# Kernel optimization log

Measured on AMD Instinct MI355X. Metric: run time of the kernel, lower is better.

The kernel has to match this reference:

```python
import jax, jax.numpy as jnp
import numpy as np

N_NODES = 100000
N_EDGES = 1600000
NUM_GRAPHS = 1000

def gcn_conv(x, edge_index, W, b, n):
    # PyG GCNConv: out = D^-1/2 (A + I) D^-1/2 (x W) + b
    xw = x @ W                                   # [n, F_out]
    loop = jnp.arange(n, dtype=edge_index.dtype)
    src = jnp.concatenate([edge_index[0], loop])  # sources (messages come from src)
    dst = jnp.concatenate([edge_index[1], loop])  # targets (aggregated into dst)
    deg = jnp.zeros((n,), xw.dtype).at[dst].add(1.0)
    dinv = jnp.where(deg > 0, jax.lax.rsqrt(deg), 0.0)
    norm = dinv[src] * dinv[dst]                  # [E+n]
    msg = xw[src] * norm[:, None]                 # gather + scale
    out = jax.ops.segment_sum(msg, dst, num_segments=n)
    return out + b

def scatter_mean(x, seg, num_segments):
    sums = jax.ops.segment_sum(x, seg, num_segments=num_segments)
    cnt = jax.ops.segment_sum(jnp.ones((x.shape[0],), x.dtype), seg, num_segments=num_segments)
    return sums / jnp.maximum(cnt, 1.0)[:, None]

def setup_inputs() -> dict:
    key = jax.random.key(0)
    ks = jax.random.split(key, 9)
    x = jax.random.normal(ks[0], (N_NODES, 256), dtype=jnp.float32)
    edge_index = jax.random.randint(ks[1], (2, N_EDGES), 0, N_NODES, dtype=jnp.int64 if jax.config.jax_enable_x64 else jnp.int32).astype(jnp.int32)
    batch = jnp.sort(jax.random.randint(ks[2], (N_NODES,), 0, NUM_GRAPHS)).astype(jnp.int32)
    W1 = jax.random.normal(ks[3], (256, 128), dtype=jnp.float32) * 0.05
    b1 = jax.random.normal(ks[4], (128,), dtype=jnp.float32) * 0.05
    W2 = jax.random.normal(ks[5], (128, 64), dtype=jnp.float32) * 0.05
    b2 = jax.random.normal(ks[6], (64,), dtype=jnp.float32) * 0.05
    fc_W = jax.random.normal(ks[7], (64, 4), dtype=jnp.float32) * 0.05
    fc_b = jax.random.normal(ks[8], (4,), dtype=jnp.float32) * 0.05
    return {"x": x, "edge_index": edge_index, "batch": batch, "W1": W1, "b1": b1, "W2": W2, "b2": b2, "fc_W": fc_W, "fc_b": fc_b}

def reference(x, edge_index, batch, W1, b1, W2, b2, fc_W, fc_b):
    n = x.shape[0]
    h = gcn_conv(x, edge_index, W1, b1, n)
    h = jax.nn.relu(h)                 # dropout p=0.0 is identity
    h = gcn_conv(h, edge_index, W2, b2, n)
    g = scatter_mean(h, batch, NUM_GRAPHS)   # [G, out_feats]
    logits = g @ fc_W + fc_b
    return jax.nn.log_softmax(logits, axis=1)
```

## Files before the change

### kernel.cpp

```cpp
#include <hip/hip_runtime.h>
#include <hip/hip_bf16.h>

#define N_NODES 100000
#define N_EDGES 1600000
#define NUM_GRAPHS 1000

#define NODES_PER_BUCKET 256
#define BUCKET_SHIFT 8
#define NBUCKETS 391
#define CAP 5120

#define G1_BLOCKS 782
#define FUSED_BLOCKS 1563
#define FILL_CHUNK 2052

typedef __attribute__((ext_vector_type(8))) short short8;
typedef __attribute__((ext_vector_type(4))) float f32x4;
typedef __attribute__((ext_vector_type(2))) float f32x2;
typedef unsigned short ushort;

__device__ __forceinline__ ushort f2bf(float f) {
    unsigned int u = __float_as_uint(f);
    u = u + 0x7fffu + ((u >> 16) & 1u);
    return (ushort)(u >> 16);
}

__device__ __forceinline__ unsigned char f2fp8(float f) {
    return (unsigned char)(__builtin_amdgcn_cvt_pk_fp8_f32(f, f, 0, false) & 0xff);
}

__global__ void setup_kernel(int* __restrict__ bcursor,
                             const float* __restrict__ W1, ushort* __restrict__ W1t,
                             const float* __restrict__ W2, ushort* __restrict__ W2t,
                             float* __restrict__ gsum, float* __restrict__ gcnt) {
    int b = blockIdx.x, tid = threadIdx.x;
    if (b < 2) {
        int i = b * 256 + tid;
        if (i < NBUCKETS) bcursor[i] = i * CAP;
    } else if (b < 130) {
        int idx = (b - 2) * 256 + tid;
        int n = idx & 127, k = idx >> 7;
        W1t[n * 256 + k] = f2bf(W1[k * 128 + n]);
    } else if (b < 162) {
        int idx = (b - 130) * 256 + tid;
        int n = idx & 63, k = idx >> 6;
        W2t[n * 128 + k] = f2bf(W2[k * 64 + n]);
    } else {
        int idx = (b - 162) * 256 + tid;
        if (idx < NUM_GRAPHS * 64) gsum[idx] = 0.f;
        else if (idx < NUM_GRAPHS * 64 + NUM_GRAPHS) gcnt[idx - NUM_GRAPHS * 64] = 0.f;
    }
}
#define SETUP_BLOCKS 416

__global__ __launch_bounds__(256) void gemm1_fill_kernel(const float* __restrict__ x,
                                                         const ushort* __restrict__ W1t,
                                                         unsigned char* __restrict__ outb,
                                                         const int* __restrict__ esrc,
                                                         const int* __restrict__ edst,
                                                         int* __restrict__ bcursor,
                                                         int* __restrict__ pairs) {
    __shared__ short8 Bs[2048];
    const int b = blockIdx.x;
    const int tid = threadIdx.x;

    if (b & 1) {
        int* scnt = (int*)Bs;
        int* spos = scnt + NBUCKETS;
        const int fid = b >> 1;
        const int beg = fid * FILL_CHUNK;
        int end = beg + FILL_CHUNK;
        if (end > N_EDGES) end = N_EDGES;
        if (beg >= end) return;
        for (int i = tid; i < NBUCKETS; i += 256) scnt[i] = 0;
        __syncthreads();
        for (int e = beg + tid * 4; e < end; e += 1024) {
            int4 d4 = *(const int4*)&edst[e];
            atomicAdd(&scnt[d4.x >> BUCKET_SHIFT], 1);
            atomicAdd(&scnt[d4.y >> BUCKET_SHIFT], 1);
            atomicAdd(&scnt[d4.z >> BUCKET_SHIFT], 1);
            atomicAdd(&scnt[d4.w >> BUCKET_SHIFT], 1);
        }
        __syncthreads();
        for (int i = tid; i < NBUCKETS; i += 256) {
            int c = scnt[i];
            spos[i] = c > 0 ? atomicAdd(&bcursor[i], c) : 0;
        }
        __syncthreads();
        for (int e = beg + tid * 4; e < end; e += 1024) {
            int4 d4 = *(const int4*)&edst[e];
            int4 s4 = *(const int4*)&esrc[e];
            int p0 = atomicAdd(&spos[d4.x >> BUCKET_SHIFT], 1);
            pairs[p0] = (s4.x << 8) | (d4.x & 255);
            int p1 = atomicAdd(&spos[d4.y >> BUCKET_SHIFT], 1);
            pairs[p1] = (s4.y << 8) | (d4.y & 255);
            int p2 = atomicAdd(&spos[d4.z >> BUCKET_SHIFT], 1);
            pairs[p2] = (s4.z << 8) | (d4.z & 255);
            int p3 = atomicAdd(&spos[d4.w >> BUCKET_SHIFT], 1);
            pairs[p3] = (s4.w << 8) | (d4.w & 255);
        }
        return;
    }

    const int gid = b >> 1;
    const int row0 = gid * 128;
    const int wv = tid >> 6;
    const int l = tid & 63;
    const int lrow = l & 15;
    const int quad = l >> 4;

    int r0 = row0 + wv * 16 + lrow;
    int r1 = r0 + 64;
    if (r0 > N_NODES - 1) r0 = N_NODES - 1;
    if (r1 > N_NODES - 1) r1 = N_NODES - 1;
    const float* xr0 = x + (size_t)r0 * 256 + quad * 8;
    const float* xr1 = x + (size_t)r1 * 256 + quad * 8;
    const int frag = lrow * 4 + quad;

    f32x4 acc[2][8];
#pragma unroll
    for (int m = 0; m < 2; ++m)
#pragma unroll
        for (int t = 0; t < 8; ++t) acc[m][t] = (f32x4){0.f, 0.f, 0.f, 0.f};

    for (int s = 0; s < 2; ++s) {
        if (s) __syncthreads();
#pragma unroll
        for (int j = 0; j < 8; ++j) {
            int slot = j * 256 + tid;
            int kcl = slot >> 9, t = (slot >> 6) & 7, lr = (slot >> 2) & 15, q = slot & 3;
            Bs[slot] = *(const short8*)(W1t + (t * 16 + lr) * 256 + (s * 4 + kcl) * 32 + q * 8);
        }
        __syncthreads();

#pragma unroll
        for (int kcl = 0; kcl < 4; ++kcl) {
            const int kc = s * 4 + kcl;
            float4 a00 = *(const float4*)(xr0 + kc * 32);
            float4 a01 = *(const float4*)(xr0 + kc * 32 + 4);
            float4 a10 = *(const float4*)(xr1 + kc * 32);
            float4 a11 = *(const float4*)(xr1 + kc * 32 + 4);
            short8 af0, af1;
            af0[0] = (short)f2bf(a00.x); af0[1] = (short)f2bf(a00.y);
            af0[2] = (short)f2bf(a00.z); af0[3] = (short)f2bf(a00.w);
            af0[4] = (short)f2bf(a01.x); af0[5] = (short)f2bf(a01.y);
            af0[6] = (short)f2bf(a01.z); af0[7] = (short)f2bf(a01.w);
            af1[0] = (short)f2bf(a10.x); af1[1] = (short)f2bf(a10.y);
            af1[2] = (short)f2bf(a10.z); af1[3] = (short)f2bf(a10.w);
            af1[4] = (short)f2bf(a11.x); af1[5] = (short)f2bf(a11.y);
            af1[6] = (short)f2bf(a11.z); af1[7] = (short)f2bf(a11.w);
#pragma unroll
            for (int t = 0; t < 8; ++t) {
                short8 bfrag = Bs[kcl * 512 + t * 64 + frag];
                acc[0][t] = __builtin_amdgcn_mfma_f32_16x16x32_bf16(af0, bfrag, acc[0][t], 0, 0, 0);
                acc[1][t] = __builtin_amdgcn_mfma_f32_16x16x32_bf16(af1, bfrag, acc[1][t], 0, 0, 0);
            }
        }
    }

#pragma unroll
    for (int m = 0; m < 2; ++m) {
        const int rbase = row0 + m * 64 + wv * 16 + quad * 4;
#pragma unroll
        for (int t = 0; t < 8; ++t) {
#pragma unroll
            for (int r = 0; r < 4; ++r) {
                int row = rbase + r;
                if (row < N_NODES)
                    outb[(size_t)row * 128 + t * 16 + lrow] = f2fp8(acc[m][t][r]);
            }
        }
    }
}

__global__ __launch_bounds__(256) void csr_fill_local_kernel(const int* __restrict__ pairs,
                                                             const int* __restrict__ bcursor,
                                                             int* __restrict__ csr_src,
                                                             int* __restrict__ row_beg,
                                                             int* __restrict__ row_end,
                                                             float* __restrict__ dinv) {
    __shared__ int plds[CAP];
    __shared__ int hist[256];
    __shared__ int scanv[256];
    __shared__ int cur[256];
    const int b = blockIdx.x;
    const int base = b * CAP;
    const int tid = threadIdx.x;
    const int cnt_b = bcursor[b] - base;

    for (int i = tid; i < cnt_b; i += 256) plds[i] = pairs[base + i];
    hist[tid] = 0;
    __syncthreads();
    for (int i = tid; i < cnt_b; i += 256) atomicAdd(&hist[plds[i] & 255], 1);
    __syncthreads();

    int deg = hist[tid];
    scanv[tid] = deg;
    for (int off = 1; off < 256; off <<= 1) {
        __syncthreads();
        int add = (tid >= off) ? scanv[tid - off] : 0;
        __syncthreads();
        scanv[tid] += add;
    }
    __syncthreads();
    int excl = scanv[tid] - deg;

    int node = b * NODES_PER_BUCKET + tid;
    if (node < N_NODES) {
        int beg = base + excl;
        row_beg[node] = beg;
        row_end[node] = beg + deg;
        dinv[node] = rsqrtf((float)(deg + 1));
    }
    cur[tid] = excl;
    __syncthreads();

    for (int i = tid; i < cnt_b; i += 256) {
        int pr = plds[i];
        int pos = base + atomicAdd(&cur[pr & 255], 1);
        csr_src[pos] = ((unsigned int)pr) >> 8;
    }
}

__global__ __launch_bounds__(256) void agg1_kernel(const unsigned int* __restrict__ xw,
                                                   const int* __restrict__ csr_src,
                                                   const int* __restrict__ row_beg,
                                                   const int* __restrict__ row_end,
                                                   const float* __restrict__ dinv,
                                                   const float* __restrict__ bias,
                                                   ushort* __restrict__ h) {
    const int wave = threadIdx.x >> 6;
    const int lane = threadIdx.x & 63;
    const int h2 = lane >> 5;
    const int c = lane & 31;
    const int node = blockIdx.x * 8 + wave * 2 + h2;

    const int beg = row_beg[node], end = row_end[node];
    const float dvn = rsqrtf((float)(end - beg + 1));

    unsigned int sv = xw[(size_t)node * 32 + c];
    f32x2 slo = __builtin_amdgcn_cvt_pk_f32_fp8(sv, false);
    f32x2 shi = __builtin_amdgcn_cvt_pk_f32_fp8(sv, true);
    float a0 = dvn * slo[0], a1 = dvn * slo[1], a2 = dvn * shi[0], a3 = dvn * shi[1];

    for (int e = beg; e < end; e += 16) {
        int s[16];
        s[0] = csr_src[e];
#pragma unroll
        for (int i = 1; i < 16; ++i)
            s[i] = (e + i < end) ? csr_src[e + i] : s[0];
        unsigned int v[16];
        float ds[16];
#pragma unroll
        for (int i = 0; i < 16; ++i) {
            v[i] = xw[(size_t)s[i] * 32 + c];
            ds[i] = dinv[s[i]];
        }
#pragma unroll
        for (int i = 0; i < 16; ++i) {
            if (i == 0 || e + i < end) {
                f32x2 lo = __builtin_amdgcn_cvt_pk_f32_fp8(v[i], false);
                f32x2 hi = __builtin_amdgcn_cvt_pk_f32_fp8(v[i], true);
                a0 += ds[i] * lo[0]; a1 += ds[i] * lo[1];
                a2 += ds[i] * hi[0]; a3 += ds[i] * hi[1];
            }
        }
    }
    float4 bv = *(const float4*)&bias[c * 4];
    float v0 = a0 * dvn + bv.x, v1 = a1 * dvn + bv.y;
    float v2 = a2 * dvn + bv.z, v3 = a3 * dvn + bv.w;
    ushort4 o;
    o.x = f2bf(v0 > 0.f ? v0 : 0.f);
    o.y = f2bf(v1 > 0.f ? v1 : 0.f);
    o.z = f2bf(v2 > 0.f ? v2 : 0.f);
    o.w = f2bf(v3 > 0.f ? v3 : 0.f);
    *(ushort4*)&h[(size_t)node * 128 + c * 4] = o;
}

__global__ __launch_bounds__(256) void gemm2_kernel(const ushort* __restrict__ h,
                                                    const ushort* __restrict__ W2t,
                                                    unsigned char* __restrict__ outb) {
    __shared__ short8 Bs[1024];
    const int tid = threadIdx.x;
    const int row0 = blockIdx.x * 128;
    const int wv = tid >> 6;
    const int l = tid & 63;
    const int lrow = l & 15;
    const int quad = l >> 4;

    int r0 = row0 + wv * 16 + lrow;
    int r1 = r0 + 64;
    if (r0 > N_NODES - 1) r0 = N_NODES - 1;
    if (r1 > N_NODES - 1) r1 = N_NODES - 1;
    const ushort* h0 = h + (size_t)r0 * 128 + quad * 8;
    const ushort* h1 = h + (size_t)r1 * 128 + quad * 8;
    const int frag = lrow * 4 + quad;

#pragma unroll
    for (int j = 0; j < 4; ++j) {
        int slot = j * 256 + tid;
        int kc = slot >> 8, t = (slot >> 6) & 3, lr = (slot >> 2) & 15, q = slot & 3;
        Bs[slot] = *(const short8*)(W2t + (t * 16 + lr) * 128 + kc * 32 + q * 8);
    }
    __syncthreads();

    f32x4 acc[2][4];
#pragma unroll
    for (int m = 0; m < 2; ++m)
#pragma unroll
        for (int t = 0; t < 4; ++t) acc[m][t] = (f32x4){0.f, 0.f, 0.f, 0.f};

#pragma unroll
    for (int kc = 0; kc < 4; ++kc) {
        short8 af0 = *(const short8*)(h0 + kc * 32);
        short8 af1 = *(const short8*)(h1 + kc * 32);
#pragma unroll
        for (int t = 0; t < 4; ++t) {
            short8 bfrag = Bs[kc * 256 + t * 64 + frag];
            acc[0][t] = __builtin_amdgcn_mfma_f32_16x16x32_bf16(af0, bfrag, acc[0][t], 0, 0, 0);
            acc[1][t] = __builtin_amdgcn_mfma_f32_16x16x32_bf16(af1, bfrag, acc[1][t], 0, 0, 0);
        }
    }

#pragma unroll
    for (int m = 0; m < 2; ++m) {
        const int rbase = row0 + m * 64 + wv * 16 + quad * 4;
#pragma unroll
        for (int r = 0; r < 4; ++r) {
            int row = rbase + r;
            if (row < N_NODES) {
#pragma unroll
                for (int t = 0; t < 4; ++t)
                    outb[(size_t)row * 64 + t * 16 + lrow] = f2fp8(acc[m][t][r]);
            }
        }
    }
}

__global__ __launch_bounds__(256) void agg2_pool_kernel(const unsigned int* __restrict__ xw,
                                                        const int* __restrict__ csr_src,
                                                        const int* __restrict__ row_beg,
                                                        const int* __restrict__ row_end,
                                                        const float* __restrict__ dinv,
                                                        const float* __restrict__ bias,
                                                        const int* __restrict__ batch,
                                                        float* __restrict__ gsum,
                                                        float* __restrict__ gcnt) {
    __shared__ float part[16][64];
    __shared__ int bsh[16];
    const int wave = threadIdx.x >> 6;
    const int lane = threadIdx.x & 63;
    const int q = lane >> 4;
    const int c = lane & 15;
    const int nl = wave * 4 + q;
    const int node = blockIdx.x * 16 + nl;

    const int beg = row_beg[node], end = row_end[node];
    const float dvn = rsqrtf((float)(end - beg + 1));

    unsigned int sv = xw[(size_t)node * 16 + c];
    f32x2 slo = __builtin_amdgcn_cvt_pk_f32_fp8(sv, false);
    f32x2 shi = __builtin_amdgcn_cvt_pk_f32_fp8(sv, true);
    float a0 = dvn * slo[0], a1 = dvn * slo[1], a2 = dvn * shi[0], a3 = dvn * shi[1];

    for (int e = beg; e < end; e += 16) {
        int s[16];
        s[0] = csr_src[e];
#pragma unroll
        for (int i = 1; i < 16; ++i)
            s[i] = (e + i < end) ? csr_src[e + i] : s[0];
        unsigned int v[16];
        float ds[16];
#pragma unroll
        for (int i = 0; i < 16; ++i) {
            v[i] = xw[(size_t)s[i] * 16 + c];
            ds[i] = dinv[s[i]];
        }
#pragma unroll
        for (int i = 0; i < 16; ++i) {
            if (i == 0 || e + i < end) {
                f32x2 lo = __builtin_amdgcn_cvt_pk_f32_fp8(v[i], false);
                f32x2 hi = __builtin_amdgcn_cvt_pk_f32_fp8(v[i], true);
                a0 += ds[i] * lo[0]; a1 += ds[i] * lo[1];
                a2 += ds[i] * hi[0]; a3 += ds[i] * hi[1];
            }
        }
    }
    float4 bv = *(const float4*)&bias[c * 4];
    float4 val = make_float4(a0 * dvn + bv.x, a1 * dvn + bv.y,
                             a2 * dvn + bv.z, a3 * dvn + bv.w);
    *(float4*)&part[nl][c * 4] = val;
    if (lane == (q << 4)) bsh[nl] = batch[node];
    __syncthreads();

    if (wave == 0) {
        int b0 = bsh[0];
        bool same = true;
#pragma unroll
        for (int i = 1; i < 16; ++i) same = same && (bsh[i] == b0);
        if (same) {
            float s = 0.f;
#pragma unroll
            for (int i = 0; i < 16; ++i) s += part[i][lane];
            atomicAdd(&gsum[b0 * 64 + lane], s);
            if (lane == 0) atomicAdd(&gcnt[b0], 16.0f);
        } else {
#pragma unroll
            for (int i = 0; i < 16; ++i)
                atomicAdd(&gsum[bsh[i] * 64 + lane], part[i][lane]);
            if (lane == 0) {
#pragma unroll
                for (int i = 0; i < 16; ++i) atomicAdd(&gcnt[bsh[i]], 1.0f);
            }
        }
    }
}

__global__ void head_kernel(const float* __restrict__ gsum, const float* __restrict__ gcnt,
                            const float* __restrict__ fcW, const float* __restrict__ fcb,
                            float* __restrict__ out) {
    int g = blockIdx.x * blockDim.x + threadIdx.x;
    if (g >= NUM_GRAPHS) return;
    float c = gcnt[g];
    c = c > 1.f ? c : 1.f;
    float inv = 1.f / c;
    float logits[4];
#pragma unroll
    for (int j = 0; j < 4; ++j) logits[j] = fcb[j];
    for (int k = 0; k < 64; ++k) {
        float m = gsum[g * 64 + k] * inv;
#pragma unroll
        for (int j = 0; j < 4; ++j) logits[j] += m * fcW[k * 4 + j];
    }
    float mx = logits[0];
#pragma unroll
    for (int j = 1; j < 4; ++j) mx = logits[j] > mx ? logits[j] : mx;
    float s = 0.f;
#pragma unroll
    for (int j = 0; j < 4; ++j) s += expf(logits[j] - mx);
    float lse = mx + logf(s);
#pragma unroll
    for (int j = 0; j < 4; ++j) out[g * 4 + j] = logits[j] - lse;
}

extern "C" void kernel_launch(void* const* d_in, const int* in_sizes, int n_in,
                              void* d_out, int out_size, void* d_ws, size_t ws_size,
                              hipStream_t stream) {
    const float* x     = (const float*)d_in[0];
    const int*   ei    = (const int*)d_in[1];
    const int*   batch = (const int*)d_in[2];
    const float* W1    = (const float*)d_in[3];
    const float* b1    = (const float*)d_in[4];
    const float* W2    = (const float*)d_in[5];
    const float* b2    = (const float*)d_in[6];
    const float* fcW   = (const float*)d_in[7];
    const float* fcb   = (const float*)d_in[8];
    float* out = (float*)d_out;

    const int* src = ei;
    const int* dst = ei + N_EDGES;

    size_t o = 0;
    char* wsb = (char*)d_ws;
    auto take = [&](size_t bytes) -> void* {
        void* p = wsb + o;
        o += (bytes + 255) & ~(size_t)255;
        return p;
    };
    float* dinv      = (float*)take((size_t)N_NODES * 4);
    int*   row_beg   = (int*)take((size_t)N_NODES * 4);
    int*   row_end   = (int*)take((size_t)N_NODES * 4);
    int*   bcursor   = (int*)take((size_t)NBUCKETS * 4);
    int*   csr_src   = (int*)take((size_t)NBUCKETS * CAP * 4);
    int*   pairs     = (int*)take((size_t)NBUCKETS * CAP * 4);
    ushort* W1t      = (ushort*)take((size_t)128 * 256 * 2);
    ushort* W2t      = (ushort*)take((size_t)64 * 128 * 2);
    unsigned char* bufA = (unsigned char*)take((size_t)N_NODES * 128);
    ushort* bufB     = (ushort*)take((size_t)N_NODES * 128 * 2);
    float* gsum      = (float*)take((size_t)NUM_GRAPHS * 64 * 4);
    float* gcnt      = (float*)take((size_t)NUM_GRAPHS * 4);
    (void)ws_size;

    const int TB = 256;

    setup_kernel<<<SETUP_BLOCKS, TB, 0, stream>>>(bcursor, W1, W1t, W2, W2t, gsum, gcnt);

    gemm1_fill_kernel<<<FUSED_BLOCKS, TB, 0, stream>>>(x, W1t, bufA, src, dst, bcursor, pairs);

    csr_fill_local_kernel<<<NBUCKETS, TB, 0, stream>>>(pairs, bcursor, csr_src,
                                                       row_beg, row_end, dinv);

    agg1_kernel<<<N_NODES / 8, TB, 0, stream>>>((const unsigned int*)bufA, csr_src,
                                                row_beg, row_end, dinv, b1, bufB);

    gemm2_kernel<<<(N_NODES + 127) / 128, TB, 0, stream>>>(bufB, W2t, bufA);

    agg2_pool_kernel<<<N_NODES / 16, TB, 0, stream>>>((const unsigned int*)bufA, csr_src,
                                                      row_beg, row_end, dinv, b2, batch,
                                                      gsum, gcnt);

    head_kernel<<<(NUM_GRAPHS + TB - 1) / TB, TB, 0, stream>>>(gsum, gcnt, fcW, fcb, out);
}
```

Baseline: 316.2 us.

## Pre-scale GEMM outputs by source dinv and compute degrees with early atomics

Node in-degrees are now counted up front with global atomics in the setup kernel, replacing the dinv array built in the CSR fill. Both GEMM epilogues multiply each output row by rsqrt(deg+1) before the fp8 store, so the aggregation kernels no longer gather dinv[src] per edge. They now just sum the pre-scaled neighbour features. The bucket-binning blocks are also regrouped into fewer, larger contiguous chunks instead of being interleaved with GEMM blocks. The cost is an extra memset and 1.6M scattered global atomics on the degree array, plus applying the scale before the fp8 quantization, which slightly changes rounding.

After: 373.4 us. 18.1% more time.

```diff
diff --git a/kernel.cpp b/kernel.cpp
--- a/kernel.cpp
+++ b/kernel.cpp
@@ -11,8 +11,12 @@
 #define CAP 5120
 
 #define G1_BLOCKS 782
-#define FUSED_BLOCKS 1563
-#define FILL_CHUNK 2052
+#define BIN_BLOCKS 196
+#define FILL_CHUNK 8192
+#define FUSED_BLOCKS (BIN_BLOCKS + G1_BLOCKS)
+
+#define DEG_BLOCKS 200
+#define DEG_CHUNK 8000
 
 typedef __attribute__((ext_vector_type(8))) short short8;
 typedef __attribute__((ext_vector_type(4))) float f32x4;
@@ -32,7 +36,8 @@
 __global__ void setup_kernel(int* __restrict__ bcursor,
                              const float* __restrict__ W1, ushort* __restrict__ W1t,
                              const float* __restrict__ W2, ushort* __restrict__ W2t,
-                             float* __restrict__ gsum, float* __restrict__ gcnt) {
+                             float* __restrict__ gsum, float* __restrict__ gcnt,
+                             const int* __restrict__ edst, int* __restrict__ deg) {
     int b = blockIdx.x, tid = threadIdx.x;
     if (b < 2) {
         int i = b * 256 + tid;
@@ -45,16 +50,29 @@
         int idx = (b - 130) * 256 + tid;
         int n = idx & 63, k = idx >> 6;
         W2t[n * 128 + k] = f2bf(W2[k * 64 + n]);
-    } else {
+    } else if (b < 416) {
         int idx = (b - 162) * 256 + tid;
         if (idx < NUM_GRAPHS * 64) gsum[idx] = 0.f;
         else if (idx < NUM_GRAPHS * 64 + NUM_GRAPHS) gcnt[idx - NUM_GRAPHS * 64] = 0.f;
-    }
-}
-#define SETUP_BLOCKS 416
+    } else {
+        const int fid = b - 416;
+        const int beg = fid * DEG_CHUNK;
+        int end = beg + DEG_CHUNK;
+        if (end > N_EDGES) end = N_EDGES;
+        for (int e = beg + tid * 4; e < end; e += 1024) {
+            int4 d4 = *(const int4*)&edst[e];
+            atomicAdd(&deg[d4.x], 1);
+            atomicAdd(&deg[d4.y], 1);
+            atomicAdd(&deg[d4.z], 1);
+            atomicAdd(&deg[d4.w], 1);
+        }
+    }
+}
+#define SETUP_BLOCKS (416 + DEG_BLOCKS)
 
 __global__ __launch_bounds__(256) void gemm1_fill_kernel(const float* __restrict__ x,
                                                          const ushort* __restrict__ W1t,
+                                                         const int* __restrict__ deg,
                                                          unsigned char* __restrict__ outb,
                                                          const int* __restrict__ esrc,
                                                          const int* __restrict__ edst,
@@ -64,11 +82,10 @@
     const int b = blockIdx.x;
     const int tid = threadIdx.x;
 
-    if (b & 1) {
+    if (b < BIN_BLOCKS) {
         int* scnt = (int*)Bs;
         int* spos = scnt + NBUCKETS;
-        const int fid = b >> 1;
-        const int beg = fid * FILL_CHUNK;
+        const int beg = b * FILL_CHUNK;
         int end = beg + FILL_CHUNK;
         if (end > N_EDGES) end = N_EDGES;
         if (beg >= end) return;
@@ -102,7 +119,7 @@
         return;
     }
 
-    const int gid = b >> 1;
+    const int gid = b - BIN_BLOCKS;
     const int row0 = gid * 128;
     const int wv = tid >> 6;
     const int l = tid & 63;
@@ -158,6 +175,17 @@
         }
     }
 
+    float sc[2][4];
+#pragma unroll
+    for (int m = 0; m < 2; ++m) {
+        const int rb = row0 + m * 64 + wv * 16 + quad * 4;
+#pragma unroll
+        for (int r = 0; r < 4; ++r) {
+            int row = rb + r;
+            int dg = (row < N_NODES) ? deg[row] : 0;
+            sc[m][r] = rsqrtf((float)(dg + 1));
+        }
+    }
 #pragma unroll
     for (int m = 0; m < 2; ++m) {
         const int rbase = row0 + m * 64 + wv * 16 + quad * 4;
@@ -167,7 +195,7 @@
             for (int r = 0; r < 4; ++r) {
                 int row = rbase + r;
                 if (row < N_NODES)
-                    outb[(size_t)row * 128 + t * 16 + lrow] = f2fp8(acc[m][t][r]);
+                    outb[(size_t)row * 128 + t * 16 + lrow] = f2fp8(sc[m][r] * acc[m][t][r]);
             }
         }
     }
@@ -177,8 +205,7 @@
                                                              const int* __restrict__ bcursor,
                                                              int* __restrict__ csr_src,
                                                              int* __restrict__ row_beg,
-                                                             int* __restrict__ row_end,
-                                                             float* __restrict__ dinv) {
+                                                             int* __restrict__ row_end) {
     __shared__ int plds[CAP];
     __shared__ int hist[256];
     __shared__ int scanv[256];
@@ -210,7 +237,6 @@
         int beg = base + excl;
         row_beg[node] = beg;
         row_end[node] = beg + deg;
-        dinv[node] = rsqrtf((float)(deg + 1));
     }
     cur[tid] = excl;
     __syncthreads();
@@ -226,7 +252,6 @@
                                                    const int* __restrict__ csr_src,
                                                    const int* __restrict__ row_beg,
                                                    const int* __restrict__ row_end,
-                                                   const float* __restrict__ dinv,
                                                    const float* __restrict__ bias,
                                                    ushort* __restrict__ h) {
     const int wave = threadIdx.x >> 6;
@@ -241,7 +266,7 @@
     unsigned int sv = xw[(size_t)node * 32 + c];
     f32x2 slo = __builtin_amdgcn_cvt_pk_f32_fp8(sv, false);
     f32x2 shi = __builtin_amdgcn_cvt_pk_f32_fp8(sv, true);
-    float a0 = dvn * slo[0], a1 = dvn * slo[1], a2 = dvn * shi[0], a3 = dvn * shi[1];
+    float a0 = slo[0], a1 = slo[1], a2 = shi[0], a3 = shi[1];
 
     for (int e = beg; e < end; e += 16) {
         int s[16];
@@ -250,19 +275,16 @@
         for (int i = 1; i < 16; ++i)
             s[i] = (e + i < end) ? csr_src[e + i] : s[0];
         unsigned int v[16];
-        float ds[16];
-#pragma unroll
-        for (int i = 0; i < 16; ++i) {
+#pragma unroll
+        for (int i = 0; i < 16; ++i)
             v[i] = xw[(size_t)s[i] * 32 + c];
-            ds[i] = dinv[s[i]];
-        }
 #pragma unroll
         for (int i = 0; i < 16; ++i) {
             if (i == 0 || e + i < end) {
                 f32x2 lo = __builtin_amdgcn_cvt_pk_f32_fp8(v[i], false);
                 f32x2 hi = __builtin_amdgcn_cvt_pk_f32_fp8(v[i], true);
-                a0 += ds[i] * lo[0]; a1 += ds[i] * lo[1];
-                a2 += ds[i] * hi[0]; a3 += ds[i] * hi[1];
+                a0 += lo[0]; a1 += lo[1];
+                a2 += hi[0]; a3 += hi[1];
             }
         }
     }
@@ -279,6 +301,7 @@
 
 __global__ __launch_bounds__(256) void gemm2_kernel(const ushort* __restrict__ h,
                                                     const ushort* __restrict__ W2t,
+                                                    const int* __restrict__ deg,
                                                     unsigned char* __restrict__ outb) {
     __shared__ short8 Bs[1024];
     const int tid = threadIdx.x;
@@ -329,9 +352,10 @@
         for (int r = 0; r < 4; ++r) {
             int row = rbase + r;
             if (row < N_NODES) {
+                float scv = rsqrtf((float)(deg[row] + 1));
 #pragma unroll
                 for (int t = 0; t < 4; ++t)
-                    outb[(size_t)row * 64 + t * 16 + lrow] = f2fp8(acc[m][t][r]);
+                    outb[(size_t)row * 64 + t * 16 + lrow] = f2fp8(scv * acc[m][t][r]);
             }
         }
     }
@@ -341,7 +365,6 @@
                                                         const int* __restrict__ csr_src,
                                                         const int* __restrict__ row_beg,
                                                         const int* __restrict__ row_end,
-                                                        const float* __restrict__ dinv,
                                                         const float* __restrict__ bias,
                                                         const int* __restrict__ batch,
                                                         float* __restrict__ gsum,
@@ -361,7 +384,7 @@
     unsigned int sv = xw[(size_t)node * 16 + c];
     f32x2 slo = __builtin_amdgcn_cvt_pk_f32_fp8(sv, false);
     f32x2 shi = __builtin_amdgcn_cvt_pk_f32_fp8(sv, true);
-    float a0 = dvn * slo[0], a1 = dvn * slo[1], a2 = dvn * shi[0], a3 = dvn * shi[1];
+    float a0 = slo[0], a1 = slo[1], a2 = shi[0], a3 = shi[1];
 
     for (int e = beg; e < end; e += 16) {
         int s[16];
@@ -370,19 +393,16 @@
         for (int i = 1; i < 16; ++i)
             s[i] = (e + i < end) ? csr_src[e + i] : s[0];
         unsigned int v[16];
-        float ds[16];
-#pragma unroll
-        for (int i = 0; i < 16; ++i) {
+#pragma unroll
+        for (int i = 0; i < 16; ++i)
             v[i] = xw[(size_t)s[i] * 16 + c];
-            ds[i] = dinv[s[i]];
-        }
 #pragma unroll
         for (int i = 0; i < 16; ++i) {
             if (i == 0 || e + i < end) {
                 f32x2 lo = __builtin_amdgcn_cvt_pk_f32_fp8(v[i], false);
                 f32x2 hi = __builtin_amdgcn_cvt_pk_f32_fp8(v[i], true);
-                a0 += ds[i] * lo[0]; a1 += ds[i] * lo[1];
-                a2 += ds[i] * hi[0]; a3 += ds[i] * hi[1];
+                a0 += lo[0]; a1 += lo[1];
+                a2 += hi[0]; a3 += hi[1];
             }
         }
     }
@@ -467,7 +487,7 @@
         o += (bytes + 255) & ~(size_t)255;
         return p;
     };
-    float* dinv      = (float*)take((size_t)N_NODES * 4);
+    int*   deg       = (int*)take((size_t)N_NODES * 4);
     int*   row_beg   = (int*)take((size_t)N_NODES * 4);
     int*   row_end   = (int*)take((size_t)N_NODES * 4);
     int*   bcursor   = (int*)take((size_t)NBUCKETS * 4);
@@ -483,20 +503,24 @@
 
     const int TB = 256;
 
-    setup_kernel<<<SETUP_BLOCKS, TB, 0, stream>>>(bcursor, W1, W1t, W2, W2t, gsum, gcnt);
-
-    gemm1_fill_kernel<<<FUSED_BLOCKS, TB, 0, stream>>>(x, W1t, bufA, src, dst, bcursor, pairs);
+    hipMemsetAsync(deg, 0, (size_t)N_NODES * 4, stream);
+
+    setup_kernel<<<SETUP_BLOCKS, TB, 0, stream>>>(bcursor, W1, W1t, W2, W2t, gsum, gcnt,
+                                                  dst, deg);
+
+    gemm1_fill_kernel<<<FUSED_BLOCKS, TB, 0, stream>>>(x, W1t, deg, bufA, src, dst,
+                                                       bcursor, pairs);
 
     csr_fill_local_kernel<<<NBUCKETS, TB, 0, stream>>>(pairs, bcursor, csr_src,
-                                                       row_beg, row_end, dinv);
+                                                       row_beg, row_end);
 
     agg1_kernel<<<N_NODES / 8, TB, 0, stream>>>((const unsigned int*)bufA, csr_src,
-                                                row_beg, row_end, dinv, b1, bufB);
-
-    gemm2_kernel<<<(N_NODES + 127) / 128, TB, 0, stream>>>(bufB, W2t, bufA);
+                                                row_beg, row_end, b1, bufB);
+
+    gemm2_kernel<<<(N_NODES + 127) / 128, TB, 0, stream>>>(bufB, W2t, deg, bufA);
 
     agg2_pool_kernel<<<N_NODES / 16, TB, 0, stream>>>((const unsigned int*)bufA, csr_src,
-                                                      row_beg, row_end, dinv, b2, batch,
+                                                      row_beg, row_end, b2, batch,
                                                       gsum, gcnt);
 
     head_kernel<<<(NUM_GRAPHS + TB - 1) / TB, TB, 0, stream>>>(gsum, gcnt, fcW, fcb, out);
```

## Store hidden activations in fp8 and preload GEMM A fragments before MMA loops

Applied to the files above, without the earlier changes.

The first-layer aggregation output h is now packed to fp8 instead of bf16, which halves the bytes written by agg1 and read by gemm2. gemm2 unpacks the fp8 values to bf16 in registers before its MFMA loop. In gemm1, all x rows are loaded and converted to bf16 up front, so global loads are issued early and overlap the W1 staging into LDS. This adds quantization error on the hidden activations and uses more registers, which could lower occupancy.

Result: no change. 310.5 us (-1.8%).

```diff
diff --git a/kernel.cpp b/kernel.cpp
--- a/kernel.cpp
+++ b/kernel.cpp
@@ -10,7 +10,6 @@
 #define NBUCKETS 391
 #define CAP 5120
 
-#define G1_BLOCKS 782
 #define FUSED_BLOCKS 1563
 #define FILL_CHUNK 2052
 
@@ -117,12 +116,33 @@
     const float* xr1 = x + (size_t)r1 * 256 + quad * 8;
     const int frag = lrow * 4 + quad;
 
+    short8 af[2][8];
+#pragma unroll
+    for (int kc = 0; kc < 8; ++kc) {
+        float4 p0 = *(const float4*)(xr0 + kc * 32);
+        float4 q0 = *(const float4*)(xr0 + kc * 32 + 4);
+        float4 p1 = *(const float4*)(xr1 + kc * 32);
+        float4 q1 = *(const float4*)(xr1 + kc * 32 + 4);
+        short8 t0, t1;
+        t0[0] = (short)f2bf(p0.x); t0[1] = (short)f2bf(p0.y);
+        t0[2] = (short)f2bf(p0.z); t0[3] = (short)f2bf(p0.w);
+        t0[4] = (short)f2bf(q0.x); t0[5] = (short)f2bf(q0.y);
+        t0[6] = (short)f2bf(q0.z); t0[7] = (short)f2bf(q0.w);
+        t1[0] = (short)f2bf(p1.x); t1[1] = (short)f2bf(p1.y);
+        t1[2] = (short)f2bf(p1.z); t1[3] = (short)f2bf(p1.w);
+        t1[4] = (short)f2bf(q1.x); t1[5] = (short)f2bf(q1.y);
+        t1[6] = (short)f2bf(q1.z); t1[7] = (short)f2bf(q1.w);
+        af[0][kc] = t0;
+        af[1][kc] = t1;
+    }
+
     f32x4 acc[2][8];
 #pragma unroll
     for (int m = 0; m < 2; ++m)
 #pragma unroll
         for (int t = 0; t < 8; ++t) acc[m][t] = (f32x4){0.f, 0.f, 0.f, 0.f};
 
+#pragma unroll
     for (int s = 0; s < 2; ++s) {
         if (s) __syncthreads();
 #pragma unroll
@@ -135,25 +155,11 @@
 
 #pragma unroll
         for (int kcl = 0; kcl < 4; ++kcl) {
-            const int kc = s * 4 + kcl;
-            float4 a00 = *(const float4*)(xr0 + kc * 32);
-            float4 a01 = *(const float4*)(xr0 + kc * 32 + 4);
-            float4 a10 = *(const float4*)(xr1 + kc * 32);
-            float4 a11 = *(const float4*)(xr1 + kc * 32 + 4);
-            short8 af0, af1;
-            af0[0] = (short)f2bf(a00.x); af0[1] = (short)f2bf(a00.y);
-            af0[2] = (short)f2bf(a00.z); af0[3] = (short)f2bf(a00.w);
-            af0[4] = (short)f2bf(a01.x); af0[5] = (short)f2bf(a01.y);
-            af0[6] = (short)f2bf(a01.z); af0[7] = (short)f2bf(a01.w);
-            af1[0] = (short)f2bf(a10.x); af1[1] = (short)f2bf(a10.y);
-            af1[2] = (short)f2bf(a10.z); af1[3] = (short)f2bf(a10.w);
-            af1[4] = (short)f2bf(a11.x); af1[5] = (short)f2bf(a11.y);
-            af1[6] = (short)f2bf(a11.z); af1[7] = (short)f2bf(a11.w);
 #pragma unroll
             for (int t = 0; t < 8; ++t) {
                 short8 bfrag = Bs[kcl * 512 + t * 64 + frag];
-                acc[0][t] = __builtin_amdgcn_mfma_f32_16x16x32_bf16(af0, bfrag, acc[0][t], 0, 0, 0);
-                acc[1][t] = __builtin_amdgcn_mfma_f32_16x16x32_bf16(af1, bfrag, acc[1][t], 0, 0, 0);
+                acc[0][t] = __builtin_amdgcn_mfma_f32_16x16x32_bf16(af[0][s * 4 + kcl], bfrag, acc[0][t], 0, 0, 0);
+                acc[1][t] = __builtin_amdgcn_mfma_f32_16x16x32_bf16(af[1][s * 4 + kcl], bfrag, acc[1][t], 0, 0, 0);
             }
         }
     }
@@ -228,7 +234,7 @@
                                                    const int* __restrict__ row_end,
                                                    const float* __restrict__ dinv,
                                                    const float* __restrict__ bias,
-                                                   ushort* __restrict__ h) {
+                                                   unsigned int* __restrict__ h) {
     const int wave = threadIdx.x >> 6;
     const int lane = threadIdx.x & 63;
     const int h2 = lane >> 5;
@@ -269,15 +275,16 @@
     float4 bv = *(const float4*)&bias[c * 4];
     float v0 = a0 * dvn + bv.x, v1 = a1 * dvn + bv.y;
     float v2 = a2 * dvn + bv.z, v3 = a3 * dvn + bv.w;
-    ushort4 o;
-    o.x = f2bf(v0 > 0.f ? v0 : 0.f);
-    o.y = f2bf(v1 > 0.f ? v1 : 0.f);
-    o.z = f2bf(v2 > 0.f ? v2 : 0.f);
-    o.w = f2bf(v3 > 0.f ? v3 : 0.f);
-    *(ushort4*)&h[(size_t)node * 128 + c * 4] = o;
-}
-
-__global__ __launch_bounds__(256) void gemm2_kernel(const ushort* __restrict__ h,
+    v0 = v0 > 0.f ? v0 : 0.f;
+    v1 = v1 > 0.f ? v1 : 0.f;
+    v2 = v2 > 0.f ? v2 : 0.f;
+    v3 = v3 > 0.f ? v3 : 0.f;
+    unsigned int o = __builtin_amdgcn_cvt_pk_fp8_f32(v0, v1, 0, false);
+    o = __builtin_amdgcn_cvt_pk_fp8_f32(v2, v3, o, true);
+    h[(size_t)node * 32 + c] = o;
+}
+
+__global__ __launch_bounds__(256) void gemm2_kernel(const unsigned char* __restrict__ h,
                                                     const ushort* __restrict__ W2t,
                                                     unsigned char* __restrict__ outb) {
     __shared__ short8 Bs[1024];
@@ -292,9 +299,36 @@
     int r1 = r0 + 64;
     if (r0 > N_NODES - 1) r0 = N_NODES - 1;
     if (r1 > N_NODES - 1) r1 = N_NODES - 1;
-    const ushort* h0 = h + (size_t)r0 * 128 + quad * 8;
-    const ushort* h1 = h + (size_t)r1 * 128 + quad * 8;
+    const unsigned char* h0 = h + (size_t)r0 * 128 + quad * 8;
+    const unsigned char* h1 = h + (size_t)r1 * 128 + quad * 8;
     const int frag = lrow * 4 + quad;
+
+    short8 af[2][4];
+#pragma unroll
+    for (int kc = 0; kc < 4; ++kc) {
+        uint2 u0 = *(const uint2*)(h0 + kc * 32);
+        uint2 u1 = *(const uint2*)(h1 + kc * 32);
+        f32x2 x0 = __builtin_amdgcn_cvt_pk_f32_fp8(u0.x, false);
+        f32x2 x1 = __builtin_amdgcn_cvt_pk_f32_fp8(u0.x, true);
+        f32x2 x2 = __builtin_amdgcn_cvt_pk_f32_fp8(u0.y, false);
+        f32x2 x3 = __builtin_amdgcn_cvt_pk_f32_fp8(u0.y, true);
+        short8 t0;
+        t0[0] = (short)f2bf(x0[0]); t0[1] = (short)f2bf(x0[1]);
+        t0[2] = (short)f2bf(x1[0]); t0[3] = (short)f2bf(x1[1]);
+        t0[4] = (short)f2bf(x2[0]); t0[5] = (short)f2bf(x2[1]);
+        t0[6] = (short)f2bf(x3[0]); t0[7] = (short)f2bf(x3[1]);
+        af[0][kc] = t0;
+        f32x2 y0 = __builtin_amdgcn_cvt_pk_f32_fp8(u1.x, false);
+        f32x2 y1 = __builtin_amdgcn_cvt_pk_f32_fp8(u1.x, true);
+        f32x2 y2 = __builtin_amdgcn_cvt_pk_f32_fp8(u1.y, false);
+        f32x2 y3 = __builtin_amdgcn_cvt_pk_f32_fp8(u1.y, true);
+        short8 t1;
+        t1[0] = (short)f2bf(y0[0]); t1[1] = (short)f2bf(y0[1]);
+        t1[2] = (short)f2bf(y1[0]); t1[3] = (short)f2bf(y1[1]);
+        t1[4] = (short)f2bf(y2[0]); t1[5] = (short)f2bf(y2[1]);
+        t1[6] = (short)f2bf(y3[0]); t1[7] = (short)f2bf(y3[1]);
+        af[1][kc] = t1;
+    }
 
 #pragma unroll
     for (int j = 0; j < 4; ++j) {
@@ -312,13 +346,11 @@
 
 #pragma unroll
     for (int kc = 0; kc < 4; ++kc) {
-        short8 af0 = *(const short8*)(h0 + kc * 32);
-        short8 af1 = *(const short8*)(h1 + kc * 32);
 #pragma unroll
         for (int t = 0; t < 4; ++t) {
             short8 bfrag = Bs[kc * 256 + t * 64 + frag];
-            acc[0][t] = __builtin_amdgcn_mfma_f32_16x16x32_bf16(af0, bfrag, acc[0][t], 0, 0, 0);
-            acc[1][t] = __builtin_amdgcn_mfma_f32_16x16x32_bf16(af1, bfrag, acc[1][t], 0, 0, 0);
+            acc[0][t] = __builtin_amdgcn_mfma_f32_16x16x32_bf16(af[0][kc], bfrag, acc[0][t], 0, 0, 0);
+            acc[1][t] = __builtin_amdgcn_mfma_f32_16x16x32_bf16(af[1][kc], bfrag, acc[1][t], 0, 0, 0);
         }
     }
 
@@ -476,7 +508,7 @@
     ushort* W1t      = (ushort*)take((size_t)128 * 256 * 2);
     ushort* W2t      = (ushort*)take((size_t)64 * 128 * 2);
     unsigned char* bufA = (unsigned char*)take((size_t)N_NODES * 128);
-    ushort* bufB     = (ushort*)take((size_t)N_NODES * 128 * 2);
+    unsigned char* bufB = (unsigned char*)take((size_t)N_NODES * 128);
     float* gsum      = (float*)take((size_t)NUM_GRAPHS * 64 * 4);
     float* gcnt      = (float*)take((size_t)NUM_GRAPHS * 4);
     (void)ws_size;
@@ -491,7 +523,8 @@
                                                        row_beg, row_end, dinv);
 
     agg1_kernel<<<N_NODES / 8, TB, 0, stream>>>((const unsigned int*)bufA, csr_src,
-                                                row_beg, row_end, dinv, b1, bufB);
+                                                row_beg, row_end, dinv, b1,
+                                                (unsigned int*)bufB);
 
     gemm2_kernel<<<(N_NODES + 127) / 128, TB, 0, stream>>>(bufB, W2t, bufA);
 
```
